# Performance work log

Hardware: AMD Instinct MI355X
Metric: run time of the kernel (lower is better)

The kernel has to match this reference:

```python
import jax, jax.numpy as jnp
import numpy as np

B, D_IN, N, L, P, C = 512, 784, 2048, 6, 15, 10  # batch, input, width, dag layers, weight pairs, classes


def setup_inputs() -> dict:
    key = jax.random.key(0)
    ks = jax.random.split(key, 10)
    x = jax.random.normal(ks[0], (B, D_IN), jnp.float32)
    w_in = jax.random.normal(ks[1], (N, D_IN), jnp.float32) * 0.1
    b_in = jax.random.normal(ks[2], (N,), jnp.float32) * 0.1
    W = jax.random.normal(ks[3], (P, N, N), jnp.float32) * 0.1
    # binary 0/1 float masks standing in for DAG connectivity masks
    M = jax.random.bernoulli(ks[4], 0.5, (P, N, N)).astype(jnp.float32)
    b = jax.random.normal(ks[5], (L - 1, N), jnp.float32) * 0.1
    w_out1 = jax.random.normal(ks[6], (C, N), jnp.float32) * 0.1
    b_out1 = jax.random.normal(ks[7], (C,), jnp.float32) * 0.1
    w_out2 = jax.random.normal(ks[8], (C, N), jnp.float32) * 0.1
    b_out2 = jax.random.normal(ks[9], (C,), jnp.float32) * 0.1
    return {"x": x, "w_in": w_in, "b_in": b_in, "W": W, "M": M, "b": b,
            "w_out1": w_out1, "b_out1": b_out1, "w_out2": w_out2, "b_out2": b_out2}


def reference(x, w_in, b_in, W, M, b, w_out1, b_out1, w_out2, b_out2):
    # input layer
    acts = [jax.nn.relu(x @ w_in.T + b_in)]  # [B, N]
    idx = 0
    for i in range(1, L):  # DAG layer i has predecessors 0..i-1
        Wm = W[idx:idx + i] * M[idx:idx + i]          # [i, N, N] masked weights
        stacked = jnp.stack(acts)                      # [i, B, N]
        # sum over predecessors of inp @ Wm.T; bias added once per predecessor
        out = jnp.einsum('jbn,jmn->bm', stacked, Wm) + i * b[i - 1]
        acts.append(jax.nn.relu(out))
        idx += i
    return acts[-1] @ w_out1.T + b_out1 + acts[-2] @ w_out2.T + b_out2
```

## Files before the change

kernel.cpp:

```cpp
#include <hip/hip_runtime.h>

typedef __bf16 bf16;
typedef __attribute__((ext_vector_type(8))) __bf16 bf16x8;
typedef __attribute__((ext_vector_type(4))) __bf16 bf16x4;
typedef __attribute__((ext_vector_type(4))) float floatx4;

#define B_SZ 512
#define N_SZ 2048
#define DIN  784
#define DINP 800
#define ACT_LD 12288

__device__ __forceinline__ void load_lds16(const bf16* g, bf16* l) {
    __builtin_amdgcn_global_load_lds(
        (const __attribute__((address_space(1))) void*)g,
        (__attribute__((address_space(3))) void*)l, 16, 0, 0);
}

__global__ __launch_bounds__(256)
void prep_kernel(const float* __restrict__ x, const float* __restrict__ w_in,
                 bf16* __restrict__ xb, bf16* __restrict__ w_inb)
{
    int g = blockIdx.x * 256 + threadIdx.x;
    const int GPR = DINP / 4;
    const float* src; bf16* dst; int row, c;
    if (g < B_SZ * GPR) {
        row = g / GPR; c = g - row * GPR;
        src = x + (size_t)row * DIN;  dst = xb + (size_t)row * DINP;
    } else {
        int h = g - B_SZ * GPR;
        row = h / GPR; c = h - row * GPR;
        src = w_in + (size_t)row * DIN;  dst = w_inb + (size_t)row * DINP;
    }
    int k = c * 4;
    floatx4 v = (floatx4){0.f, 0.f, 0.f, 0.f};
    if (k < DIN) v = *(const floatx4*)(src + k);
    bf16x4 o;
    o[0] = (bf16)v[0]; o[1] = (bf16)v[1]; o[2] = (bf16)v[2]; o[3] = (bf16)v[3];
    *(bf16x4*)(dst + k) = o;
}

__global__ __launch_bounds__(256, 2)
void gemm_kernel(const bf16* __restrict__ A, int lda,
                 const bf16* __restrict__ Bm, int ldb,
                 float* __restrict__ partial,
                 int chunkK, int Ktot)
{
    __shared__ bf16 As[128 * 32];
    __shared__ bf16 Bs[128 * 32];

    const int t    = threadIdx.x;
    const int lane = t & 63, wave = t >> 6;
    const int wm   = (wave & 1) * 64, wn = (wave >> 1) * 64;
    const int l15  = lane & 15, quad = lane >> 4;
    const int n0   = blockIdx.x * 128, m0 = blockIdx.y * 128;
    const int s    = blockIdx.z;
    const int kb   = s * chunkK;
    const int ke   = (kb + chunkK < Ktot) ? (kb + chunkK) : Ktot;

    const int rA = wave * 16 + (lane >> 2);
    const int cA = (lane & 3) * 8;
    const bf16* pA0 = A  + (size_t)(m0 + rA) * lda + cA + kb;
    const bf16* pA1 = pA0 + (size_t)64 * lda;
    const bf16* pB0 = Bm + (size_t)(n0 + rA) * ldb + cA + kb;
    const bf16* pB1 = pB0 + (size_t)64 * ldb;
    bf16* dA0 = &As[wave * 512];  bf16* dA1 = &As[(wave + 4) * 512];
    bf16* dB0 = &Bs[wave * 512];  bf16* dB1 = &Bs[(wave + 4) * 512];

    floatx4 acc[4][4];
#pragma unroll
    for (int a = 0; a < 4; a++)
#pragma unroll
        for (int b = 0; b < 4; b++) acc[a][b] = (floatx4){0.f, 0.f, 0.f, 0.f};

    for (int k0 = kb; k0 < ke; k0 += 32) {
        __syncthreads();
        load_lds16(pA0, dA0);  load_lds16(pA1, dA1);
        load_lds16(pB0, dB0);  load_lds16(pB1, dB1);
        pA0 += 32; pA1 += 32; pB0 += 32; pB1 += 32;
        __syncthreads();

        bf16x8 af[4], bfr[4];
#pragma unroll
        for (int a = 0; a < 4; a++)
            af[a] = *(const bf16x8*)(&As[(wm + a * 16 + l15) * 32 + quad * 8]);
#pragma unroll
        for (int b = 0; b < 4; b++)
            bfr[b] = *(const bf16x8*)(&Bs[(wn + b * 16 + l15) * 32 + quad * 8]);
#pragma unroll
        for (int a = 0; a < 4; a++)
#pragma unroll
            for (int b = 0; b < 4; b++)
                acc[a][b] = __builtin_amdgcn_mfma_f32_16x16x32_bf16(af[a], bfr[b], acc[a][b], 0, 0, 0);
    }

    float* outp = partial + (size_t)s * (B_SZ * N_SZ);
#pragma unroll
    for (int a = 0; a < 4; a++)
#pragma unroll
        for (int b = 0; b < 4; b++)
#pragma unroll
            for (int r = 0; r < 4; r++) {
                int row = m0 + wm + a * 16 + quad * 4 + r;
                int col = n0 + wn + b * 16 + l15;
                outp[(size_t)row * N_SZ + col] = acc[a][b][r];
            }
}

__global__ __launch_bounds__(512, 2)
void dag_gemm_kernel(const bf16* __restrict__ A,
                     const float* __restrict__ Wl, const float* __restrict__ Ml,
                     float* __restrict__ partial,
                     int chunkK)
{
    __shared__ bf16 Bs[2][4096];

    const int t    = threadIdx.x;
    const int lane = t & 63, wave = t >> 6;
    const int l15  = lane & 15, quad = lane >> 4;
    const int n0   = (blockIdx.x >> 3) * 64;
    const int z    = blockIdx.x & 7;
    const int kb   = z * chunkK;
    const int nt   = chunkK >> 6;

    const int br = t >> 3, bc = (t & 7) * 8;
    const size_t wrow = (size_t)(n0 + br) << 11;
    bf16* bdst = &Bs[0][br * 64 + (bc ^ ((br & 7) << 3))];

    const bf16* Abase = A + (size_t)(wave * 64 + l15) * ACT_LD + quad * 8 + kb;

    floatx4 acc[4][4];
#pragma unroll
    for (int a = 0; a < 4; a++)
#pragma unroll
        for (int b = 0; b < 4; b++) acc[a][b] = (floatx4){0.f, 0.f, 0.f, 0.f};

    floatx4 w0a, w1a, m0a, m1a;
    floatx4 w0b, w1b, m0b, m1b;
    bf16x8 af0[8], af1[8];

#define LOAD_WM(tt, w0, w1, m0, m1) do {                          \
        int k = kb + (tt) * 64;                                   \
        int jj = k >> 11, kk2 = k & 2047;                         \
        size_t o = ((size_t)jj << 22) + wrow + kk2 + bc;          \
        w0 = *(const floatx4*)(Wl + o);                           \
        w1 = *(const floatx4*)(Wl + o + 4);                       \
        m0 = *(const floatx4*)(Ml + o);                           \
        m1 = *(const floatx4*)(Ml + o + 4);                       \
    } while (0)

#define COMMIT(buf, w0, w1, m0, m1) do {                          \
        bf16x8 o8;                                                \
        o8[0] = (bf16)(w0[0] * m0[0]); o8[1] = (bf16)(w0[1] * m0[1]); \
        o8[2] = (bf16)(w0[2] * m0[2]); o8[3] = (bf16)(w0[3] * m0[3]); \
        o8[4] = (bf16)(w1[0] * m1[0]); o8[5] = (bf16)(w1[1] * m1[1]); \
        o8[6] = (bf16)(w1[2] * m1[2]); o8[7] = (bf16)(w1[3] * m1[3]); \
        *(bf16x8*)(bdst + (buf) * 4096) = o8;                     \
    } while (0)

#define BAR() do {                                                \
        asm volatile("s_waitcnt lgkmcnt(0)" ::: "memory");        \
        __builtin_amdgcn_s_barrier();                             \
    } while (0)

    auto loadA = [&](bf16x8* af, int tt) {
        const bf16* ap = Abase + tt * 64;
#pragma unroll
        for (int a = 0; a < 4; a++) {
            af[a]     = *(const bf16x8*)(ap + (size_t)(a * 16) * ACT_LD);
            af[4 + a] = *(const bf16x8*)(ap + (size_t)(a * 16) * ACT_LD + 32);
        }
    };
    auto mma = [&](int buf, const bf16x8* af) {
#pragma unroll
        for (int kk = 0; kk < 2; kk++) {
            const int e = (kk * 32 + quad * 8) ^ ((l15 & 7) << 3);
            bf16x8 bfr[4];
#pragma unroll
            for (int b = 0; b < 4; b++)
                bfr[b] = *(const bf16x8*)(&Bs[buf][(b * 16 + l15) * 64 + e]);
#pragma unroll
            for (int a = 0; a < 4; a++)
#pragma unroll
                for (int b = 0; b < 4; b++)
                    acc[a][b] = __builtin_amdgcn_mfma_f32_16x16x32_bf16(
                        af[kk * 4 + a], bfr[b], acc[a][b], 0, 0, 0);
        }
    };

    LOAD_WM(0, w0a, w1a, m0a, m1a);
    LOAD_WM(1, w0b, w1b, m0b, m1b);
    loadA(af0, 0);
    COMMIT(0, w0a, w1a, m0a, m1a);
    LOAD_WM(2, w0a, w1a, m0a, m1a);
    loadA(af1, 1);
    BAR();

    for (int tt = 0; tt < nt; tt += 2) {
        COMMIT(1, w0b, w1b, m0b, m1b);
        if (tt + 3 < nt) LOAD_WM(tt + 3, w0b, w1b, m0b, m1b);
        mma(0, af0);
        if (tt + 2 < nt) loadA(af0, tt + 2);
        BAR();
        if (tt + 2 < nt) COMMIT(0, w0a, w1a, m0a, m1a);
        if (tt + 4 < nt) LOAD_WM(tt + 4, w0a, w1a, m0a, m1a);
        mma(1, af1);
        if (tt + 3 < nt) loadA(af1, tt + 3);
        BAR();
    }
#undef LOAD_WM
#undef COMMIT
#undef BAR

    float* outp = partial + (size_t)z * (B_SZ * N_SZ);
#pragma unroll
    for (int a = 0; a < 4; a++)
#pragma unroll
        for (int b = 0; b < 4; b++)
#pragma unroll
            for (int r = 0; r < 4; r++) {
                int row = wave * 64 + a * 16 + quad * 4 + r;
                int col = n0 + b * 16 + l15;
                outp[(size_t)row * N_SZ + col] = acc[a][b][r];
            }
}

__global__ __launch_bounds__(256)
void epilogue_kernel(const float* __restrict__ partial, int S,
                     const float* __restrict__ bias, float bscale,
                     bf16* __restrict__ actdst)
{
    int g = blockIdx.x * 256 + threadIdx.x;
    size_t off = (size_t)g * 4;
    int b = (int)(off >> 11);
    int n = (int)(off & (N_SZ - 1));
    floatx4 v = *(const floatx4*)(partial + off);
    for (int s2 = 1; s2 < S; s2++)
        v += *(const floatx4*)(partial + (size_t)s2 * (B_SZ * N_SZ) + off);
    floatx4 bv = *(const floatx4*)(bias + n);
    bf16x4 o;
#pragma unroll
    for (int j = 0; j < 4; j++) {
        float xv = v[j] + bscale * bv[j];
        xv = xv > 0.f ? xv : 0.f;
        o[j] = (bf16)xv;
    }
    *(bf16x4*)(actdst + (size_t)b * ACT_LD + n) = o;
}

__global__ __launch_bounds__(64)
void out_kernel(const bf16* __restrict__ act4, const bf16* __restrict__ act5,
                const float* __restrict__ w1, const float* __restrict__ b1,
                const float* __restrict__ w2, const float* __restrict__ b2,
                float* __restrict__ out)
{
    int b = blockIdx.x, lane = threadIdx.x;
    float a5[32], a4[32];
#pragma unroll
    for (int rep = 0; rep < 4; rep++) {
        bf16x8 v5 = *(const bf16x8*)(act5 + (size_t)b * ACT_LD + rep * 512 + lane * 8);
        bf16x8 v4 = *(const bf16x8*)(act4 + (size_t)b * ACT_LD + rep * 512 + lane * 8);
#pragma unroll
        for (int j = 0; j < 8; j++) {
            a5[rep * 8 + j] = (float)v5[j];
            a4[rep * 8 + j] = (float)v4[j];
        }
    }
    for (int c = 0; c < 10; c++) {
        float d = 0.f;
#pragma unroll
        for (int rep = 0; rep < 4; rep++) {
            floatx4 wa = *(const floatx4*)(w1 + (size_t)c * N_SZ + rep * 512 + lane * 8);
            floatx4 wb = *(const floatx4*)(w1 + (size_t)c * N_SZ + rep * 512 + lane * 8 + 4);
            floatx4 va = *(const floatx4*)(w2 + (size_t)c * N_SZ + rep * 512 + lane * 8);
            floatx4 vb = *(const floatx4*)(w2 + (size_t)c * N_SZ + rep * 512 + lane * 8 + 4);
#pragma unroll
            for (int j = 0; j < 4; j++) {
                d += a5[rep * 8 + j] * wa[j] + a4[rep * 8 + j] * va[j];
                d += a5[rep * 8 + 4 + j] * wb[j] + a4[rep * 8 + 4 + j] * vb[j];
            }
        }
        for (int off = 32; off > 0; off >>= 1) d += __shfl_down(d, off);
        if (lane == 0) out[b * 10 + c] = d + b1[c] + b2[c];
    }
}

extern "C" void kernel_launch(void* const* d_in, const int* in_sizes, int n_in,
                              void* d_out, int out_size, void* d_ws, size_t ws_size,
                              hipStream_t stream)
{
    const float* x    = (const float*)d_in[0];
    const float* w_in = (const float*)d_in[1];
    const float* b_in = (const float*)d_in[2];
    const float* W    = (const float*)d_in[3];
    const float* M    = (const float*)d_in[4];
    const float* bL   = (const float*)d_in[5];
    const float* w1   = (const float*)d_in[6];
    const float* b1   = (const float*)d_in[7];
    const float* w2   = (const float*)d_in[8];
    const float* b2   = (const float*)d_in[9];
    float* out = (float*)d_out;

    char* ws = (char*)d_ws;
    bf16*  xb      = (bf16*)ws;
    bf16*  w_inb   = (bf16*)(ws + 819200);
    bf16*  actsT   = (bf16*)(ws + 4096000);
    float* partial = (float*)(ws + 16678912);

    prep_kernel<<<2000, 256, 0, stream>>>(x, w_in, xb, w_inb);

    gemm_kernel<<<dim3(16, 4, 4), 256, 0, stream>>>(
        xb, DINP, w_inb, DINP, partial, 224, DINP);
    epilogue_kernel<<<1024, 256, 0, stream>>>(partial, 4, b_in, 1.0f, actsT);

    for (int i = 1; i < 6; i++) {
        int idx = i * (i - 1) / 2;
        const float* Wl = W + ((size_t)idx << 22);
        const float* Ml = M + ((size_t)idx << 22);
        dag_gemm_kernel<<<256, 512, 0, stream>>>(
            actsT, Wl, Ml, partial, 256 * i);
        epilogue_kernel<<<1024, 256, 0, stream>>>(
            partial, 8, bL + (size_t)(i - 1) * N_SZ, (float)i,
            actsT + (size_t)i * N_SZ);
    }

    out_kernel<<<512, 64, 0, stream>>>(
        actsT + (size_t)4 * N_SZ, actsT + (size_t)5 * N_SZ,
        w1, b1, w2, b2, out);
}
```

Baseline: 641.7 us.

## Deepen DAG GEMM pipeline to four LDS buffers with two tiles per barrier

The masked-weight GEMM now keeps four LDS buffers instead of two and runs two K-tiles of MFMA work between each barrier. It also keeps four tiles of W/M global loads in flight in registers. The aim is to halve the barrier count and hide more global-load latency behind the matrix math. In exchange it uses more registers and LDS, which under launch bounds of two 512-thread blocks may cause spills or lower occupancy. It also assumes the tile count is a multiple of four.

Result: slower. 662.6 us (+3.3%).

```diff
diff --git a/kernel.cpp b/kernel.cpp
--- a/kernel.cpp
+++ b/kernel.cpp
@@ -113,7 +113,7 @@
                      float* __restrict__ partial,
                      int chunkK)
 {
-    __shared__ bf16 Bs[2][4096];
+    __shared__ bf16 Bs[4][4096];
 
     const int t    = threadIdx.x;
     const int lane = t & 63, wave = t >> 6;
@@ -135,11 +135,13 @@
 #pragma unroll
         for (int b = 0; b < 4; b++) acc[a][b] = (floatx4){0.f, 0.f, 0.f, 0.f};
 
-    floatx4 w0a, w1a, m0a, m1a;
-    floatx4 w0b, w1b, m0b, m1b;
+    floatx4 aw0, aw1, am0, am1;
+    floatx4 bw0, bw1, bm0, bm1;
+    floatx4 cw0, cw1, cm0, cm1;
+    floatx4 dw0, dw1, dm0, dm1;
     bf16x8 af0[8], af1[8];
 
-#define LOAD_WM(tt, w0, w1, m0, m1) do {                          \
+#define LOAD1(tt, w0, w1, m0, m1) do {                            \
         int k = kb + (tt) * 64;                                   \
         int jj = k >> 11, kk2 = k & 2047;                         \
         size_t o = ((size_t)jj << 22) + wrow + kk2 + bc;          \
@@ -149,7 +151,7 @@
         m1 = *(const floatx4*)(Ml + o + 4);                       \
     } while (0)
 
-#define COMMIT(buf, w0, w1, m0, m1) do {                          \
+#define PC(buf, w0, w1, m0, m1) do {                              \
         bf16x8 o8;                                                \
         o8[0] = (bf16)(w0[0] * m0[0]); o8[1] = (bf16)(w0[1] * m0[1]); \
         o8[2] = (bf16)(w0[2] * m0[2]); o8[3] = (bf16)(w0[3] * m0[3]); \
@@ -188,28 +190,49 @@
         }
     };
 
-    LOAD_WM(0, w0a, w1a, m0a, m1a);
-    LOAD_WM(1, w0b, w1b, m0b, m1b);
-    loadA(af0, 0);
-    COMMIT(0, w0a, w1a, m0a, m1a);
-    LOAD_WM(2, w0a, w1a, m0a, m1a);
-    loadA(af1, 1);
+    LOAD1(0, aw0, aw1, am0, am1);
+    LOAD1(1, bw0, bw1, bm0, bm1);
+    loadA(af0, 0);  loadA(af1, 1);
+    PC(0, aw0, aw1, am0, am1);
+    PC(1, bw0, bw1, bm0, bm1);
+    LOAD1(2, aw0, aw1, am0, am1);
+    LOAD1(3, bw0, bw1, bm0, bm1);
+    if (nt > 4) {
+        LOAD1(4, cw0, cw1, cm0, cm1);
+        LOAD1(5, dw0, dw1, dm0, dm1);
+    }
     BAR();
 
-    for (int tt = 0; tt < nt; tt += 2) {
-        COMMIT(1, w0b, w1b, m0b, m1b);
-        if (tt + 3 < nt) LOAD_WM(tt + 3, w0b, w1b, m0b, m1b);
+    for (int t0 = 0; t0 < nt; t0 += 4) {
+        PC(2, aw0, aw1, am0, am1);
+        PC(3, bw0, bw1, bm0, bm1);
+        if (t0 + 6 < nt) {
+            LOAD1(t0 + 6, aw0, aw1, am0, am1);
+            LOAD1(t0 + 7, bw0, bw1, bm0, bm1);
+        }
         mma(0, af0);
-        if (tt + 2 < nt) loadA(af0, tt + 2);
+        mma(1, af1);
+        loadA(af0, t0 + 2);
+        loadA(af1, t0 + 3);
         BAR();
-        if (tt + 2 < nt) COMMIT(0, w0a, w1a, m0a, m1a);
-        if (tt + 4 < nt) LOAD_WM(tt + 4, w0a, w1a, m0a, m1a);
-        mma(1, af1);
-        if (tt + 3 < nt) loadA(af1, tt + 3);
+        if (t0 + 4 < nt) {
+            PC(0, cw0, cw1, cm0, cm1);
+            PC(1, dw0, dw1, dm0, dm1);
+        }
+        if (t0 + 8 < nt) {
+            LOAD1(t0 + 8, cw0, cw1, cm0, cm1);
+            LOAD1(t0 + 9, dw0, dw1, dm0, dm1);
+        }
+        mma(2, af0);
+        mma(3, af1);
+        if (t0 + 4 < nt) {
+            loadA(af0, t0 + 4);
+            loadA(af1, t0 + 5);
+        }
         BAR();
     }
-#undef LOAD_WM
-#undef COMMIT
+#undef LOAD1
+#undef PC
 #undef BAR
 
     float* outp = partial + (size_t)z * (B_SZ * N_SZ);
```
